# Optimization experiments

Hardware: AMD Instinct MI355X
Metric: run time of the kernel (lower is better)

## Reference

```python
import jax, jax.numpy as jnp
import numpy as np

A0 = 0.5291772105638411
KE = 14.399645351950548
KEHALF = KE / 2.0

def softplus_inverse(x):
    x = np.asarray(x, dtype=np.float64)
    return np.float32(x + np.log(-np.expm1(-x)))

def setup_inputs() -> dict:
    key = jax.random.key(0)
    k1, k2, k3, k4 = jax.random.split(key, 4)
    B, N, K = 16, 8192, 128
    neighbors = jax.random.randint(k1, (B, N, K), 0, N, dtype=jnp.int64)
    neighbor_mask = jnp.ones((B, N, K), dtype=jnp.float32)
    # atomic numbers in [1, 94] (Z=0 would break d/dp of Z**p)
    atomic_numbers = jax.random.randint(k2, (B, N), 0, 94, dtype=jnp.int64) + 1
    # distances scaled into a physical range [0.5, 5.5) Angstrom to avoid r->0
    distances = jax.random.uniform(k3, (B, N, K), dtype=jnp.float32) * 5.0 + 0.5
    p = lambda v: jnp.full((1,), softplus_inverse(v), dtype=jnp.float32)
    return {
        'neighbors': neighbors,
        'neighbor_mask': neighbor_mask,
        'atomic_numbers': atomic_numbers,
        'distances': distances,
        'adiv': p(1.0 / (0.8854 * A0)),
        'apow': p(0.23),
        'c1': p(0.1818), 'c2': p(0.5099), 'c3': p(0.2802), 'c4': p(0.02817),
        'a1': p(3.2), 'a2': p(0.9423), 'a3': p(0.4028), 'a4': p(0.2016),
    }

def reference(neighbors, neighbor_mask, atomic_numbers, distances,
              adiv, apow, c1, c2, c3, c4, a1, a2, a3, a4):
    sp = jax.nn.softplus
    Zf = atomic_numbers.astype(jnp.float32)            # [B, N]
    zpow = Zf ** sp(apow)                              # [B, N]
    # per-batch gather over neighbor index (sparse edge list, no NxN build)
    gather = jax.vmap(lambda v, nb: v[nb])             # ([N],[N,K]) -> [N,K]
    zpow_j = gather(zpow, neighbors)                   # [B, N, K]
    a = (zpow[:, :, None] + zpow_j) * sp(adiv) * neighbor_mask
    zizj = Zf[:, :, None] * gather(Zf, neighbors) * neighbor_mask
    c1s, c2s, c3s, c4s = sp(c1), sp(c2), sp(c3), sp(c4)
    csum = c1s + c2s + c3s + c4s
    f = (c1s / csum) * jnp.exp(-sp(a1) * a * distances) \
      + (c2s / csum) * jnp.exp(-sp(a2) * a * distances) \
      + (c3s / csum) * jnp.exp(-sp(a3) * a * distances) \
      + (c4s / csum) * jnp.exp(-sp(a4) * a * distances)
    corr = jnp.where(neighbor_mask != 0,
                     KEHALF * f * zizj / distances,
                     jnp.zeros_like(distances))        # [B, N, K]
    return jnp.sum(corr, axis=(-1, -2))[:, None]       # [B, 1]
```

## Files before the change

kernel.cpp:

```cpp
#include <hip/hip_runtime.h>


#define KEHALF_F 7.199822675975274f
#define LOG2E_F  1.4426950408889634f
#define DEPTH    4
#define GRAN     64
#define WPB      8
#define SLOTB    768

__device__ __forceinline__ float softplus_f(float x) {
    return (x > 20.f) ? x : log1pf(__expf(x));
}

__global__ void zbl_pre(const int* __restrict__ zn,
                        const float* __restrict__ adiv,
                        const float* __restrict__ apow,
                        const float* __restrict__ c1, const float* __restrict__ c2,
                        const float* __restrict__ c3, const float* __restrict__ c4,
                        const float* __restrict__ a1, const float* __restrict__ a2,
                        const float* __restrict__ a3, const float* __restrict__ a4,
                        unsigned short* __restrict__ packed, float* __restrict__ scal,
                        int total_atoms)
{
    int i = blockIdx.x * blockDim.x + threadIdx.x;
    const float spa = softplus_f(apow[0]);
    const float sad = softplus_f(adiv[0]);
    const float qb  = sad;
    const float qmax = sad * __expf(spa * __logf(94.f));
    const float qs  = (qmax - qb) * (1.f / 511.f);
    if (i == 0) {
        float s1 = softplus_f(c1[0]), s2 = softplus_f(c2[0]);
        float s3 = softplus_f(c3[0]), s4 = softplus_f(c4[0]);
        float inv = KEHALF_F / (s1 + s2 + s3 + s4);
        float w1 = s1 * inv, w2 = s2 * inv, w3 = s3 * inv, w4 = s4 * inv;
        scal[0] = sad;
        scal[1] = w1; scal[2] = w2; scal[3] = w3; scal[4] = w4;
        scal[5] = -softplus_f(a1[0]) * LOG2E_F;
        scal[6] = -softplus_f(a2[0]) * LOG2E_F;
        scal[7] = -softplus_f(a3[0]) * LOG2E_F;
        scal[8] = -softplus_f(a4[0]) * LOG2E_F;
        scal[9]  = qb;
        scal[10] = qs;
        scal[11] = __log2f(w1);
        scal[12] = __log2f(w2);
        scal[13] = __log2f(w3);
        scal[14] = __log2f(w4);
    }
    if (i < total_atoms) {
        unsigned int Z = (unsigned int)zn[i];
        float Zf = (float)Z;
        float zps = sad * __expf(spa * __logf(Zf));
        float qf = (zps - qb) / qs;
        int q = (int)(qf + 0.5f);
        if (q < 0) q = 0;
        if (q > 511) q = 511;
        packed[i] = (unsigned short)(((unsigned)q << 7) | (Z & 0x7Fu));
    }
}

extern __shared__ unsigned short tab[];

#define STAGE1(slotp, it) do {                                                    \
    const char* _g = (lane < 16) ? (const char*)(nb_ + ((it) << 6))               \
                   : (lane < 32) ? (const char*)(mk_ + ((it) << 6))               \
                                 : (const char*)(ds_ + ((it) << 6));              \
    _g += (lane & 15) * 16;                                                       \
    if (lane < 48)                                                                \
        __builtin_amdgcn_global_load_lds(                                         \
            (const __attribute__((address_space(1))) void*)_g,                    \
            (__attribute__((address_space(3))) void*)(slotp), 16, 0, 0);          \
} while (0)

#define CONSUME(sp, it) do {                                                      \
    const int   ji = *(const int*)  ((sp) + (lane << 2));                         \
    const float mm = *(const float*)((sp) + 256 + (lane << 2));                   \
    const float dd = *(const float*)((sp) + 512 + (lane << 2));                   \
    const int r = rw + ((it) << 6) + lane;                                        \
    const unsigned int wi_ = tab[r >> kshift];                                    \
    const unsigned int wj_ = tab[ji];                                             \
    const float zpi = fmaf((float)(wi_ >> 7), qs, qb);                            \
    const float Zi  = (float)(wi_ & 0x7Fu);                                       \
    const float zpj = fmaf((float)(wj_ >> 7), qs, qb);                            \
    const float Zj  = (float)(wj_ & 0x7Fu);                                       \
    const float zz = Zi * Zj * mm;                                                \
    const float ad = (zpi + zpj) * (mm * dd);                                     \
    const float f = exp2f(fmaf(e1, ad, l1)) + exp2f(fmaf(e2, ad, l2))             \
                  + exp2f(fmaf(e3, ad, l3)) + exp2f(fmaf(e4, ad, l4));            \
    acc += f * zz * __builtin_amdgcn_rcpf(dd);                                    \
} while (0)

__global__ __launch_bounds__(512, 8) void zbl_main8(
        const int*            __restrict__ neighbors,
        const float*          __restrict__ mask,
        const float*          __restrict__ dist,
        const unsigned short* __restrict__ packed,
        const float*          __restrict__ scal,
        float*                __restrict__ out,
        int N, int kshift, int epb, int iters)
{
    __shared__ char stage[WPB][DEPTH][SLOTB];

    const int tid  = threadIdx.x;
    const int w    = tid >> 6;
    const int lane = tid & 63;
    const int b    = blockIdx.y;

    const int rw = (blockIdx.x * WPB + w) * (iters * GRAN);
    const size_t ebase = (size_t)b * epb + (size_t)rw;
    const int*   nb_ = neighbors + ebase;
    const float* mk_ = mask      + ebase;
    const float* ds_ = dist      + ebase;

    const uint4* s4 = (const uint4*)(packed + (size_t)b * N);
    const int n8 = N >> 3;
    uint4 tv0, tv1;
    const bool h0 = (tid < n8);
    const bool h1 = (tid + 512 < n8);
    if (h0) tv0 = s4[tid];
    if (h1) tv1 = s4[tid + 512];

    {
        char* sp0 = &stage[w][0][0]; STAGE1(sp0, 0);
        char* sp1 = &stage[w][1][0]; STAGE1(sp1, 1);
        char* sp2 = &stage[w][2][0]; STAGE1(sp2, 2);
        char* sp3 = &stage[w][3][0]; STAGE1(sp3, 3);
    }

    {
        uint4* t4 = (uint4*)tab;
        if (h0) t4[tid] = tv0;
        if (h1) t4[tid + 512] = tv1;
    }
    const float e1 = scal[5],  e2 = scal[6],  e3 = scal[7],  e4 = scal[8];
    const float qb = scal[9],  qs = scal[10];
    const float l1 = scal[11], l2 = scal[12], l3 = scal[13], l4 = scal[14];
    __syncthreads();

    float acc = 0.f;
    int it = 0;

    for (; it < iters - DEPTH; ++it) {
        asm volatile("s_waitcnt vmcnt(3)" ::: "memory");
        char* sp = &stage[w][it & (DEPTH - 1)][0];
        const int   ji = *(const int*)  (sp + (lane << 2));
        const float mm = *(const float*)(sp + 256 + (lane << 2));
        const float dd = *(const float*)(sp + 512 + (lane << 2));
        asm volatile("s_waitcnt lgkmcnt(0)" ::: "memory");
        STAGE1(sp, it + DEPTH);
        const int r = rw + (it << 6) + lane;
        const unsigned int wi_ = tab[r >> kshift];
        const unsigned int wj_ = tab[ji];
        const float zpi = fmaf((float)(wi_ >> 7), qs, qb);
        const float Zi  = (float)(wi_ & 0x7Fu);
        const float zpj = fmaf((float)(wj_ >> 7), qs, qb);
        const float Zj  = (float)(wj_ & 0x7Fu);
        const float zz = Zi * Zj * mm;
        const float ad = (zpi + zpj) * (mm * dd);
        const float f = exp2f(fmaf(e1, ad, l1)) + exp2f(fmaf(e2, ad, l2))
                      + exp2f(fmaf(e3, ad, l3)) + exp2f(fmaf(e4, ad, l4));
        acc += f * zz * __builtin_amdgcn_rcpf(dd);
    }

    {
        asm volatile("s_waitcnt vmcnt(3)" ::: "memory");
        char* sp = &stage[w][it & (DEPTH - 1)][0];
        CONSUME(sp, it); ++it;
    }
    {
        asm volatile("s_waitcnt vmcnt(2)" ::: "memory");
        char* sp = &stage[w][it & (DEPTH - 1)][0];
        CONSUME(sp, it); ++it;
    }
    {
        asm volatile("s_waitcnt vmcnt(1)" ::: "memory");
        char* sp = &stage[w][it & (DEPTH - 1)][0];
        CONSUME(sp, it); ++it;
    }
    {
        asm volatile("s_waitcnt vmcnt(0)" ::: "memory");
        char* sp = &stage[w][it & (DEPTH - 1)][0];
        CONSUME(sp, it); ++it;
    }

    #pragma unroll
    for (int off = 32; off > 0; off >>= 1) acc += __shfl_down(acc, off);
    __syncthreads();
    float* wred = (float*)&stage[0][0][0];
    if (lane == 0) wred[w] = acc;
    __syncthreads();
    if (tid == 0) {
        float t = 0.f;
        #pragma unroll
        for (int i = 0; i < WPB; ++i) t += wred[i];
        atomicAdd(&out[b], t);
    }
}

__global__ void zbl_fallback(const int* __restrict__ neighbors,
                             const float* __restrict__ mask,
                             const float* __restrict__ dist,
                             const unsigned short* __restrict__ packed,
                             const float* __restrict__ scal,
                             float* __restrict__ out,
                             int N, int K, int epb, int total_edges)
{
    const int e = blockIdx.x * blockDim.x + threadIdx.x;
    if (e >= total_edges) return;
    const float w1 = scal[1], w2 = scal[2], w3 = scal[3], w4 = scal[4];
    const float e1 = scal[5], e2 = scal[6], e3 = scal[7], e4 = scal[8];
    const float qb = scal[9], qs = scal[10];
    const int b = e / epb;
    const int n = (e - b * epb) / K;
    const unsigned int wi = packed[(size_t)b * N + n];
    const unsigned int wj = packed[(size_t)b * N + neighbors[e]];
    const float zpi = fmaf((float)(wi >> 7), qs, qb);
    const float zpj = fmaf((float)(wj >> 7), qs, qb);
    const float Zi = (float)(wi & 0x7Fu), Zj = (float)(wj & 0x7Fu);
    const float m = mask[e], d = dist[e];
    const float a  = (zpi + zpj) * m;
    const float ad = a * d;
    const float f = w1 * exp2f(e1 * ad) + w2 * exp2f(e2 * ad)
                  + w3 * exp2f(e3 * ad) + w4 * exp2f(e4 * ad);
    const float corr = (m != 0.f) ? (f * Zi * Zj * m / d) : 0.f;
    if (corr != 0.f) atomicAdd(&out[b], corr);
}

extern "C" void kernel_launch(void* const* d_in, const int* in_sizes, int n_in,
                              void* d_out, int out_size, void* d_ws, size_t ws_size,
                              hipStream_t stream) {
    const int*   neighbors = (const int*)  d_in[0];
    const float* nb_mask   = (const float*)d_in[1];
    const int*   zn        = (const int*)  d_in[2];
    const float* dist      = (const float*)d_in[3];
    const float* adiv = (const float*)d_in[4];
    const float* apow = (const float*)d_in[5];
    const float* c1 = (const float*)d_in[6];
    const float* c2 = (const float*)d_in[7];
    const float* c3 = (const float*)d_in[8];
    const float* c4 = (const float*)d_in[9];
    const float* a1 = (const float*)d_in[10];
    const float* a2 = (const float*)d_in[11];
    const float* a3 = (const float*)d_in[12];
    const float* a4 = (const float*)d_in[13];

    const int total_edges = in_sizes[0];
    const int total_atoms = in_sizes[2];
    const int B = out_size;
    const int N = total_atoms / B;
    const int K = total_edges / total_atoms;
    const int epb = N * K;

    float*          scal   = (float*)d_ws;
    unsigned short* packed = (unsigned short*)((char*)d_ws + 64);

    hipMemsetAsync(d_out, 0, (size_t)out_size * sizeof(float), stream);

    {
        const int threads = 256;
        const int blocks = (total_atoms + threads - 1) / threads;
        zbl_pre<<<blocks, threads, 0, stream>>>(zn, adiv, apow, c1, c2, c3, c4,
                                                a1, a2, a3, a4,
                                                packed, scal, total_atoms);
    }

    int kshift = 0;
    while ((1 << kshift) < K && kshift < 30) kshift++;
    const bool kpow2 = ((1 << kshift) == K);

    const int ITERS = 32;
    const int span_block = WPB * GRAN * ITERS;
    const size_t lds_dyn = (size_t)N * 2;
    const bool fast = kpow2 && (N % 8 == 0) && (N <= 8192) &&
                      (epb % span_block == 0) &&
                      ((size_t)(64 + (size_t)total_atoms * 2) <= ws_size);
    if (fast) {
        const int bpb = epb / span_block;
        dim3 grid(bpb, B);
        zbl_main8<<<grid, 512, lds_dyn, stream>>>(
            neighbors, nb_mask, dist, packed, scal, (float*)d_out,
            N, kshift, epb, ITERS);
    } else {
        const int threads = 256;
        const int blocks = (total_edges + threads - 1) / threads;
        zbl_fallback<<<blocks, threads, 0, stream>>>(
            neighbors, nb_mask, dist, packed, scal, (float*)d_out,
            N, K, epb, total_edges);
    }
}
```

Baseline: 51.75 us.

## Replace four-exponential screening sum with LDS linear-interpolation lookup table

```diff
diff --git a/kernel.cpp b/kernel.cpp
--- a/kernel.cpp
+++ b/kernel.cpp
@@ -3,10 +3,12 @@
 
 #define KEHALF_F 7.199822675975274f
 #define LOG2E_F  1.4426950408889634f
-#define DEPTH    4
+#define DEPTH    2
 #define GRAN     64
 #define WPB      8
 #define SLOTB    768
+#define LUTN     1024
+#define LUT_ADMAX 80.0f
 
 __device__ __forceinline__ float softplus_f(float x) {
     return (x > 20.f) ? x : log1pf(__expf(x));
@@ -58,7 +60,31 @@
     }
 }
 
-extern __shared__ unsigned short tab[];
+__global__ void zbl_lut_k(const float* __restrict__ c1, const float* __restrict__ c2,
+                          const float* __restrict__ c3, const float* __restrict__ c4,
+                          const float* __restrict__ a1, const float* __restrict__ a2,
+                          const float* __restrict__ a3, const float* __restrict__ a4,
+                          float* __restrict__ lut)
+{
+    int i = blockIdx.x * blockDim.x + threadIdx.x;
+    if (i >= LUTN) return;
+    float s1 = softplus_f(c1[0]), s2 = softplus_f(c2[0]);
+    float s3 = softplus_f(c3[0]), s4 = softplus_f(c4[0]);
+    float inv = KEHALF_F / (s1 + s2 + s3 + s4);
+    float w1 = s1 * inv, w2 = s2 * inv, w3 = s3 * inv, w4 = s4 * inv;
+    float g1 = -softplus_f(a1[0]), g2 = -softplus_f(a2[0]);
+    float g3 = -softplus_f(a3[0]), g4 = -softplus_f(a4[0]);
+    const float h = LUT_ADMAX / (float)(LUTN - 1);
+    float x0 = (float)i * h, x1 = x0 + h;
+    float f0 = w1 * __expf(g1 * x0) + w2 * __expf(g2 * x0)
+             + w3 * __expf(g3 * x0) + w4 * __expf(g4 * x0);
+    float f1 = w1 * __expf(g1 * x1) + w2 * __expf(g2 * x1)
+             + w3 * __expf(g3 * x1) + w4 * __expf(g4 * x1);
+    lut[i] = f0;
+    lut[LUTN + i] = f1 - f0;
+}
+
+extern __shared__ char smem[];
 
 #define STAGE1(slotp, it) do {                                                    \
     const char* _g = (lane < 16) ? (const char*)(nb_ + ((it) << 6))               \
@@ -84,22 +110,29 @@
     const float Zj  = (float)(wj_ & 0x7Fu);                                       \
     const float zz = Zi * Zj * mm;                                                \
     const float ad = (zpi + zpj) * (mm * dd);                                     \
-    const float f = exp2f(fmaf(e1, ad, l1)) + exp2f(fmaf(e2, ad, l2))             \
-                  + exp2f(fmaf(e3, ad, l3)) + exp2f(fmaf(e4, ad, l4));            \
+    float t = fminf(ad * lscale, 1023.0f);                                        \
+    const int   li = (int)t;                                                      \
+    const float fr = t - (float)li;                                               \
+    const float f  = fmaf(fr, lutD[li], lutF[li]);                                \
     acc += f * zz * __builtin_amdgcn_rcpf(dd);                                    \
 } while (0)
 
-__global__ __launch_bounds__(512, 8) void zbl_main8(
+__global__ __launch_bounds__(512, 8) void zbl_main10(
         const int*            __restrict__ neighbors,
         const float*          __restrict__ mask,
         const float*          __restrict__ dist,
         const unsigned short* __restrict__ packed,
+        const float*          __restrict__ lutg,
         const float*          __restrict__ scal,
         float*                __restrict__ out,
         int N, int kshift, int epb, int iters)
 {
     __shared__ char stage[WPB][DEPTH][SLOTB];
 
+    unsigned short* tab  = (unsigned short*)smem;
+    float*          lutF = (float*)(smem + (size_t)N * 2);
+    float*          lutD = lutF + LUTN;
+
     const int tid  = threadIdx.x;
     const int w    = tid >> 6;
     const int lane = tid & 63;
@@ -112,35 +145,36 @@
     const float* ds_ = dist      + ebase;
 
     const uint4* s4 = (const uint4*)(packed + (size_t)b * N);
+    const uint4* l4 = (const uint4*)lutg;
     const int n8 = N >> 3;
-    uint4 tv0, tv1;
+    uint4 tv0, tv1, tv2;
     const bool h0 = (tid < n8);
     const bool h1 = (tid + 512 < n8);
     if (h0) tv0 = s4[tid];
     if (h1) tv1 = s4[tid + 512];
+    tv2 = l4[tid];
 
     {
         char* sp0 = &stage[w][0][0]; STAGE1(sp0, 0);
         char* sp1 = &stage[w][1][0]; STAGE1(sp1, 1);
-        char* sp2 = &stage[w][2][0]; STAGE1(sp2, 2);
-        char* sp3 = &stage[w][3][0]; STAGE1(sp3, 3);
     }
 
     {
         uint4* t4 = (uint4*)tab;
         if (h0) t4[tid] = tv0;
         if (h1) t4[tid + 512] = tv1;
-    }
-    const float e1 = scal[5],  e2 = scal[6],  e3 = scal[7],  e4 = scal[8];
-    const float qb = scal[9],  qs = scal[10];
-    const float l1 = scal[11], l2 = scal[12], l3 = scal[13], l4 = scal[14];
+        uint4* u4 = (uint4*)lutF;
+        u4[tid] = tv2;
+    }
+    const float qb = scal[9], qs = scal[10];
+    const float lscale = (float)(LUTN - 1) * (1.0f / LUT_ADMAX);
     __syncthreads();
 
     float acc = 0.f;
     int it = 0;
 
     for (; it < iters - DEPTH; ++it) {
-        asm volatile("s_waitcnt vmcnt(3)" ::: "memory");
+        asm volatile("s_waitcnt vmcnt(1)" ::: "memory");
         char* sp = &stage[w][it & (DEPTH - 1)][0];
         const int   ji = *(const int*)  (sp + (lane << 2));
         const float mm = *(const float*)(sp + 256 + (lane << 2));
@@ -156,21 +190,13 @@
         const float Zj  = (float)(wj_ & 0x7Fu);
         const float zz = Zi * Zj * mm;
         const float ad = (zpi + zpj) * (mm * dd);
-        const float f = exp2f(fmaf(e1, ad, l1)) + exp2f(fmaf(e2, ad, l2))
-                      + exp2f(fmaf(e3, ad, l3)) + exp2f(fmaf(e4, ad, l4));
+        float t = fminf(ad * lscale, 1023.0f);
+        const int   li = (int)t;
+        const float fr = t - (float)li;
+        const float f  = fmaf(fr, lutD[li], lutF[li]);
         acc += f * zz * __builtin_amdgcn_rcpf(dd);
     }
 
-    {
-        asm volatile("s_waitcnt vmcnt(3)" ::: "memory");
-        char* sp = &stage[w][it & (DEPTH - 1)][0];
-        CONSUME(sp, it); ++it;
-    }
-    {
-        asm volatile("s_waitcnt vmcnt(2)" ::: "memory");
-        char* sp = &stage[w][it & (DEPTH - 1)][0];
-        CONSUME(sp, it); ++it;
-    }
     {
         asm volatile("s_waitcnt vmcnt(1)" ::: "memory");
         char* sp = &stage[w][it & (DEPTH - 1)][0];
@@ -206,9 +232,9 @@
 {
     const int e = blockIdx.x * blockDim.x + threadIdx.x;
     if (e >= total_edges) return;
-    const float w1 = scal[1], w2 = scal[2], w3 = scal[3], w4 = scal[4];
     const float e1 = scal[5], e2 = scal[6], e3 = scal[7], e4 = scal[8];
     const float qb = scal[9], qs = scal[10];
+    const float l1 = scal[11], l2 = scal[12], l3 = scal[13], l4 = scal[14];
     const int b = e / epb;
     const int n = (e - b * epb) / K;
     const unsigned int wi = packed[(size_t)b * N + n];
@@ -217,10 +243,9 @@
     const float zpj = fmaf((float)(wj >> 7), qs, qb);
     const float Zi = (float)(wi & 0x7Fu), Zj = (float)(wj & 0x7Fu);
     const float m = mask[e], d = dist[e];
-    const float a  = (zpi + zpj) * m;
-    const float ad = a * d;
-    const float f = w1 * exp2f(e1 * ad) + w2 * exp2f(e2 * ad)
-                  + w3 * exp2f(e3 * ad) + w4 * exp2f(e4 * ad);
+    const float ad = (zpi + zpj) * (m * d);
+    const float f = exp2f(fmaf(e1, ad, l1)) + exp2f(fmaf(e2, ad, l2))
+                  + exp2f(fmaf(e3, ad, l3)) + exp2f(fmaf(e4, ad, l4));
     const float corr = (m != 0.f) ? (f * Zi * Zj * m / d) : 0.f;
     if (corr != 0.f) atomicAdd(&out[b], corr);
 }
@@ -252,6 +277,8 @@
 
     float*          scal   = (float*)d_ws;
     unsigned short* packed = (unsigned short*)((char*)d_ws + 64);
+    const size_t lut_off = (64 + (size_t)total_atoms * 2 + 15) & ~(size_t)15;
+    float*          lutg   = (float*)((char*)d_ws + lut_off);
 
     hipMemsetAsync(d_out, 0, (size_t)out_size * sizeof(float), stream);
 
@@ -262,6 +289,7 @@
                                                 a1, a2, a3, a4,
                                                 packed, scal, total_atoms);
     }
+    zbl_lut_k<<<LUTN / 256, 256, 0, stream>>>(c1, c2, c3, c4, a1, a2, a3, a4, lutg);
 
     int kshift = 0;
     while ((1 << kshift) < K && kshift < 30) kshift++;
@@ -269,15 +297,15 @@
 
     const int ITERS = 32;
     const int span_block = WPB * GRAN * ITERS;
-    const size_t lds_dyn = (size_t)N * 2;
+    const size_t lds_dyn = (size_t)N * 2 + (size_t)2 * LUTN * 4;
     const bool fast = kpow2 && (N % 8 == 0) && (N <= 8192) &&
                       (epb % span_block == 0) &&
-                      ((size_t)(64 + (size_t)total_atoms * 2) <= ws_size);
+                      (lut_off + 2 * LUTN * 4 <= ws_size);
     if (fast) {
         const int bpb = epb / span_block;
         dim3 grid(bpb, B);
-        zbl_main8<<<grid, 512, lds_dyn, stream>>>(
-            neighbors, nb_mask, dist, packed, scal, (float*)d_out,
+        zbl_main10<<<grid, 512, lds_dyn, stream>>>(
+            neighbors, nb_mask, dist, packed, lutg, scal, (float*)d_out,
             N, kshift, epb, ITERS);
     } else {
         const int threads = 256;
```

New measurement: 62.00 us. 1.2x slower.
